# Performance work log

Hardware: AMD Instinct MI355X
Metric: run time of the kernel (lower is better)

## Reference

```python
import jax, jax.numpy as jnp
import numpy as np

N_NODES = 20000
N_EDGES = 320000
N_GRAPHS = 32
IN_CH = 5
HID = 64
HEADS = 4
DH = HID // HEADS  # 16
LAYERS = 8
EPS = 1e-5
SLOPE = 0.2


def setup_inputs() -> dict:
    key = jax.random.key(0)
    ks = jax.random.split(key, 32)
    inp = {}
    inp['x1'] = jax.random.normal(ks[0], (N_NODES, IN_CH), dtype=jnp.float32)
    inp['x2'] = jax.random.normal(ks[1], (N_NODES, IN_CH), dtype=jnp.float32)
    inp['edge_index1'] = jax.random.randint(ks[2], (2, N_EDGES), 0, N_NODES, dtype=jnp.int32)
    inp['edge_index2'] = jax.random.randint(ks[3], (2, N_EDGES), 0, N_NODES, dtype=jnp.int32)
    inp['batch1'] = jnp.sort(jax.random.randint(ks[4], (N_NODES,), 0, N_GRAPHS, dtype=jnp.int32))
    inp['batch2'] = jnp.sort(jax.random.randint(ks[5], (N_NODES,), 0, N_GRAPHS, dtype=jnp.int32))
    # node_lin
    inp['Wn'] = jax.random.normal(ks[6], (IN_CH, HID), dtype=jnp.float32) / np.sqrt(IN_CH)
    inp['bnode'] = jnp.zeros((HID,), dtype=jnp.float32)
    # GATv2 layers (stacked over LAYERS)
    s = 1.0 / np.sqrt(HID)
    inp['Wl'] = jax.random.normal(ks[7], (LAYERS, HID, HID), dtype=jnp.float32) * s
    inp['bl'] = jnp.zeros((LAYERS, HID), dtype=jnp.float32)
    inp['Wr'] = jax.random.normal(ks[8], (LAYERS, HID, HID), dtype=jnp.float32) * s
    inp['br'] = jnp.zeros((LAYERS, HID), dtype=jnp.float32)
    inp['att'] = jax.random.normal(ks[9], (LAYERS, HEADS, DH), dtype=jnp.float32) / np.sqrt(DH)
    inp['cbias'] = jnp.zeros((LAYERS, HID), dtype=jnp.float32)
    # batch norms
    inp['gamma'] = jnp.ones((LAYERS, HID), dtype=jnp.float32)
    inp['beta'] = jnp.zeros((LAYERS, HID), dtype=jnp.float32)
    # fc head
    inp['f1w'] = jax.random.normal(ks[10], (2 * HID, 256), dtype=jnp.float32) / np.sqrt(2 * HID)
    inp['f1b'] = jnp.zeros((256,), dtype=jnp.float32)
    inp['f2w'] = jax.random.normal(ks[11], (256, 128), dtype=jnp.float32) / np.sqrt(256)
    inp['f2b'] = jnp.zeros((128,), dtype=jnp.float32)
    inp['f3w'] = jax.random.normal(ks[12], (128, 1), dtype=jnp.float32) / np.sqrt(128)
    inp['f3b'] = jnp.zeros((1,), dtype=jnp.float32)
    return inp


def _gatv2_layer(x, src, dst, Wl, bl, Wr, br, att, bias):
    # x: [N, HID]; src/dst: [E'] (self loops included)
    N = x.shape[0]
    xl = (x @ Wl + bl).reshape(N, HEADS, DH)  # source transform
    xr = (x @ Wr + br).reshape(N, HEADS, DH)  # target transform
    e = jax.nn.leaky_relu(xl[src] + xr[dst], SLOPE)          # [E, H, DH]
    score = jnp.einsum('ehd,hd->eh', e, att)                  # [E, H]
    smax = jax.ops.segment_max(score, dst, num_segments=N)    # [N, H]
    ex = jnp.exp(score - smax[dst])
    denom = jax.ops.segment_sum(ex, dst, num_segments=N)
    alpha = ex / denom[dst]                                   # [E, H]
    msg = alpha[:, :, None] * xl[src]                         # [E, H, DH]
    out = jax.ops.segment_sum(msg, dst, num_segments=N)       # [N, H, DH]
    return out.reshape(N, HID) + bias


def _forward_once(x, edge_index, batch, Wn, bnode, Wl, bl, Wr, br, att, cbias, gamma, beta):
    N = x.shape[0]
    loop = jnp.arange(N, dtype=edge_index.dtype)
    src = jnp.concatenate([edge_index[0], loop])  # add_self_loops=True
    dst = jnp.concatenate([edge_index[1], loop])
    h = x @ Wn + bnode
    for l in range(LAYERS):
        g = _gatv2_layer(h, src, dst, Wl[l], bl[l], Wr[l], br[l], att[l], cbias[l])
        mu = g.mean(axis=0)
        var = g.var(axis=0)
        g = (g - mu) / jnp.sqrt(var + EPS) * gamma[l] + beta[l]
        h = h + jax.nn.elu(g)
    # global_mean_pool
    sums = jax.ops.segment_sum(h, batch, num_segments=N_GRAPHS)
    cnt = jax.ops.segment_sum(jnp.ones((N,), dtype=h.dtype), batch, num_segments=N_GRAPHS)
    return sums / jnp.maximum(cnt, 1.0)[:, None]


def reference(x1, edge_index1, batch1, x2, edge_index2, batch2, Wn, bnode, Wl, bl, Wr, br, att, cbias, gamma, beta, f1w, f1b, f2w, f2b, f3w, f3b):
    o1 = _forward_once(x1, edge_index1, batch1, Wn, bnode, Wl, bl, Wr, br, att, cbias, gamma, beta)
    o2 = _forward_once(x2, edge_index2, batch2, Wn, bnode, Wl, bl, Wr, br, att, cbias, gamma, beta)
    c = jnp.concatenate([o1, o2], axis=1)           # [G, 128]
    h = jax.nn.relu(c @ f1w + f1b)                   # dropout = identity (eval)
    h = jax.nn.relu(h @ f2w + f2b)
    return h @ f3w + f3b                             # [G, 1]
```

## Files before the change

### kernel.cpp

```cpp
#include <hip/hip_runtime.h>
#include <hip/hip_bf16.h>
#include <hip/hip_fp16.h>

#define N_NODES 20000
#define HID 64
#define EPS 1e-5f

struct GP {
    const int* ei;
    const int* batch;
    const float* x;
    int* deg;
    int* cursor;
    int* csr;
    float* h;
    __half* xlh;
    float* xr;
    float* gb;
    float* stats;
    float* osum;
};


__global__ void k_csr_init(GP a, GP b, int n, int two) {
    int t = blockIdx.x * blockDim.x + threadIdx.x;
    if (t < n) {
        a.deg[t] = 1;
        if (two) b.deg[t] = 1;
    }
}

__global__ void k_count(GP a, GP b, int Ea, int Eb, int two) {
    int t = blockIdx.x * blockDim.x + threadIdx.x;
    if (t < Ea) atomicAdd(&a.deg[a.ei[Ea + t]], 1);
    if (two && t < Eb) atomicAdd(&b.deg[b.ei[Eb + t]], 1);
}

#define SCAN_T 1024
#define SCAN_C 20
__global__ __launch_bounds__(1024) void k_scan(GP a, GP b, int n, int totA, int totB) {
    GP g = blockIdx.x ? b : a;
    int total = blockIdx.x ? totB : totA;
    __shared__ int sd[SCAN_T];
    int t = threadIdx.x;
    int base = t * SCAN_C;
    int loc[SCAN_C];
    int s = 0;
#pragma unroll
    for (int i = 0; i < SCAN_C; ++i) {
        int idx = base + i;
        loc[i] = (idx < n) ? g.deg[idx] : 0;
        s += loc[i];
    }
    sd[t] = s;
    __syncthreads();
    for (int off = 1; off < SCAN_T; off <<= 1) {
        int v = (t >= off) ? sd[t - off] : 0;
        __syncthreads();
        sd[t] += v;
        __syncthreads();
    }
    int run = sd[t] - s;
#pragma unroll
    for (int i = 0; i < SCAN_C; ++i) {
        int idx = base + i;
        if (idx < n) { g.deg[idx] = run; g.cursor[idx] = run; run += loc[i]; }
    }
    if (t == 0) g.deg[n] = total;
}

__global__ void k_scatter(GP a, GP b, int Ea, int Eb, int n, int two) {
    int t = blockIdx.x * blockDim.x + threadIdx.x;
    if (t < Ea) {
        int s = a.ei[t], d = a.ei[Ea + t];
        a.csr[atomicAdd(&a.cursor[d], 1)] = s;
    } else if (t < Ea + n) {
        int nn = t - Ea;
        a.csr[atomicAdd(&a.cursor[nn], 1)] = nn;
    }
    if (two) {
        if (t < Eb) {
            int s = b.ei[t], d = b.ei[Eb + t];
            b.csr[atomicAdd(&b.cursor[d], 1)] = s;
        } else if (t < Eb + n) {
            int nn = t - Eb;
            b.csr[atomicAdd(&b.cursor[nn], 1)] = nn;
        }
    }
}


__global__ void k_nodelin(GP a, GP b, int nPer, const float* __restrict__ Wn,
                          const float* __restrict__ bn, int n) {
    int bid = blockIdx.x;
    GP g = a;
    if (bid >= nPer) { g = b; bid -= nPer; }
    int idx = bid * 256 + threadIdx.x;
    if (idx >= n * HID) return;
    int node = idx >> 6, c = idx & 63;
    float acc = bn[c];
#pragma unroll
    for (int k = 0; k < 5; ++k) acc += g.x[node * 5 + k] * Wn[k * HID + c];
    g.h[idx] = acc;
}


__global__ __launch_bounds__(256) void k_lin2(GP ga, GP gbp, int nPer, int n,
        const float* __restrict__ Wl, const float* __restrict__ bl,
        const float* __restrict__ Wr, const float* __restrict__ br,
        const float* __restrict__ gamma, const float* __restrict__ beta, int layer) {
    __shared__ float wls[4096], wrs[4096];
    __shared__ float hs[2048];
    int bid = blockIdx.x;
    GP g = ga;
    if (bid >= nPer) { g = gbp; bid -= nPer; }
    {
        const float4* wl4 = (const float4*)Wl;
        const float4* wr4 = (const float4*)Wr;
        float4* l4 = (float4*)wls;
        float4* r4 = (float4*)wrs;
        for (int i = threadIdx.x; i < 1024; i += 256) { l4[i] = wl4[i]; r4[i] = wr4[i]; }
    }
    int c = threadIdx.x & 63;
    int wid = threadIdx.x >> 6;
    float blv = bl[c], brv = br[c];
    float mu = 0.f, inv = 1.f, gam = 1.f, bet = 0.f;
    if (layer > 0) {
        const float* st = g.stats + (layer - 1) * 128;
        float invn = 1.0f / (float)n;
        mu = st[c] * invn;
        float var = st[64 + c] * invn - mu * mu;
        inv = rsqrtf(fmaxf(var, 0.f) + EPS);
        gam = gamma[c]; bet = beta[c];
    }
    __syncthreads();
    float* hw = &hs[wid * 512];
    const float4* hw4 = (const float4*)hw;
    for (int base = bid * 32; base < n; base += nPer * 32) {
        int nb = base + wid * 8;
        size_t off0 = (size_t)nb * 64 + c;
        float hv[8];
        if (layer > 0) {
#pragma unroll
            for (int j = 0; j < 8; ++j) {
                float gv = g.gb[off0 + j * 64];
                float ov = g.h[off0 + j * 64];
                float v = (gv - mu) * inv * gam + bet;
                v = v > 0.f ? v : expm1f(v);
                hv[j] = ov + v;
                g.h[off0 + j * 64] = hv[j];
            }
        } else {
#pragma unroll
            for (int j = 0; j < 8; ++j) hv[j] = g.h[off0 + j * 64];
        }
#pragma unroll
        for (int j = 0; j < 8; ++j) hw[j * 64 + c] = hv[j];
        float accl[8], accr[8];
#pragma unroll
        for (int j = 0; j < 8; ++j) { accl[j] = blv; accr[j] = brv; }
        for (int k4 = 0; k4 < 16; ++k4) {
            float4 hq[8];
#pragma unroll
            for (int j = 0; j < 8; ++j) hq[j] = hw4[j * 16 + k4];
#pragma unroll
            for (int kk = 0; kk < 4; ++kk) {
                float wl = wls[(k4 * 4 + kk) * 64 + c];
                float wr = wrs[(k4 * 4 + kk) * 64 + c];
#pragma unroll
                for (int j = 0; j < 8; ++j) {
                    float hx = (&hq[j].x)[kk];
                    accl[j] = fmaf(hx, wl, accl[j]);
                    accr[j] = fmaf(hx, wr, accr[j]);
                }
            }
        }
#pragma unroll
        for (int j = 0; j < 8; ++j) {
            g.xlh[off0 + j * 64] = __float2half(accl[j]);
            g.xr[off0 + j * 64] = accr[j];
        }
    }
}


__device__ __forceinline__ float red16(float p) {
    p += __int_as_float(__builtin_amdgcn_update_dpp(0, __float_as_int(p), 0xB1, 0xF, 0xF, true));
    p += __int_as_float(__builtin_amdgcn_update_dpp(0, __float_as_int(p), 0x4E, 0xF, 0xF, true));
    p += __int_as_float(__builtin_amdgcn_update_dpp(0, __float_as_int(p), 0x141, 0xF, 0xF, true));
    p += __int_as_float(__builtin_amdgcn_update_dpp(0, __float_as_int(p), 0x140, 0xF, 0xF, true));
    return p;
}

__global__ __launch_bounds__(1024) void k_attn(GP ga, GP gbp, int nPer,
        const float* __restrict__ att, const float* __restrict__ cbias, int layer, int n) {
    int bid = blockIdx.x;
    GP g = (bid & 1) ? gbp : ga;
    bid >>= 1;
    int lane = threadIdx.x & 63;
    int wid = threadIdx.x >> 6;
    int gw = bid * 16 + wid;
    int nw = nPer * 16;
    float attv = att[lane];
    float attv2 = attv * 0.2f;
    float cb = cbias[lane];
    const int* __restrict__ rowptr = g.deg;
    const int* __restrict__ csr = g.csr;
    const __half* __restrict__ xl = g.xlh;
    const float* __restrict__ xr = g.xr;
    float* __restrict__ gbuf = g.gb;
    float* st = g.stats + layer * 128;
    float bsum = 0.f, bsq = 0.f;
    for (int node = gw; node < n; node += nw) {
        int start = rowptr[node], end = rowptr[node + 1];
        float xrv = xr[(size_t)node * 64 + lane];
        float xself = __half2float(xl[(size_t)node * 64 + lane]);
        float ts = xself + xrv;
        float sself = red16(ts * (ts > 0.f ? attv : attv2));
        float lsum = 0.f, acc = 0.f;
        int idx = start;
        for (; idx + 8 <= end; idx += 8) {
            int sidx[8];
            float xv[8];
#pragma unroll
            for (int j = 0; j < 8; ++j) sidx[j] = csr[idx + j];
#pragma unroll
            for (int j = 0; j < 8; ++j) xv[j] = __half2float(xl[(size_t)sidx[j] * 64 + lane]);
#pragma unroll
            for (int j = 0; j < 8; ++j) {
                float t = xv[j] + xrv;
                float p = red16(t * (t > 0.f ? attv : attv2));
                float w = __expf(fminf(p - sself, 80.f));
                lsum += w;
                acc = fmaf(w, xv[j], acc);
            }
        }
        for (; idx + 4 <= end; idx += 4) {
            int sidx[4];
            float xv[4];
#pragma unroll
            for (int j = 0; j < 4; ++j) sidx[j] = csr[idx + j];
#pragma unroll
            for (int j = 0; j < 4; ++j) xv[j] = __half2float(xl[(size_t)sidx[j] * 64 + lane]);
#pragma unroll
            for (int j = 0; j < 4; ++j) {
                float t = xv[j] + xrv;
                float p = red16(t * (t > 0.f ? attv : attv2));
                float w = __expf(fminf(p - sself, 80.f));
                lsum += w;
                acc = fmaf(w, xv[j], acc);
            }
        }
        for (; idx < end; ++idx) {
            int s0 = csr[idx];
            float x0 = __half2float(xl[(size_t)s0 * 64 + lane]);
            float t0 = x0 + xrv;
            float p0 = red16(t0 * (t0 > 0.f ? attv : attv2));
            float w0 = __expf(fminf(p0 - sself, 80.f));
            lsum += w0;
            acc = fmaf(w0, x0, acc);
        }
        float outv = acc / lsum + cb;
        gbuf[(size_t)node * 64 + lane] = outv;
        bsum += outv; bsq += outv * outv;
    }
    __shared__ float sred[1024];
    sred[threadIdx.x] = bsum;
    __syncthreads();
    if (threadIdx.x < 64) {
        float t = 0.f;
#pragma unroll
        for (int w = 0; w < 16; ++w) t += sred[w * 64 + threadIdx.x];
        atomicAdd(&st[threadIdx.x], t);
    }
    __syncthreads();
    sred[threadIdx.x] = bsq;
    __syncthreads();
    if (threadIdx.x < 64) {
        float t = 0.f;
#pragma unroll
        for (int w = 0; w < 16; ++w) t += sred[w * 64 + threadIdx.x];
        atomicAdd(&st[64 + threadIdx.x], t);
    }
}


__global__ __launch_bounds__(256) void k_pool(GP ga, GP gbp, int nPer,
        const float* __restrict__ gamma, const float* __restrict__ beta, int n) {
    int bid = blockIdx.x;
    GP g = ga;
    if (bid >= nPer) { g = gbp; bid -= nPer; }
    int lane = threadIdx.x & 63, w = threadIdx.x >> 6;
    const float* st = g.stats + 7 * 128;
    float invn = 1.f / (float)n;
    float mu = st[lane] * invn;
    float var = st[64 + lane] * invn - mu * mu;
    float inv = rsqrtf(fmaxf(var, 0.f) + EPS);
    float gam = gamma[lane], bet = beta[lane];
    int chunk = (n + nPer - 1) / nPer;
    int s = bid * chunk;
    int e = min(s + chunk, n);
    float acc = 0.f;
    int cur = -1;
    for (int node = s + w; node < e; node += 4) {
        int bg = g.batch[node];
        size_t off = (size_t)node * 64 + lane;
        float gv = g.gb[off];
        float hv = g.h[off];
        float v = (gv - mu) * inv * gam + bet;
        float hn = hv + (v > 0.f ? v : expm1f(v));
        if (bg != cur) {
            if (cur >= 0) atomicAdd(&g.osum[cur * 64 + lane], acc);
            acc = 0.f; cur = bg;
        }
        acc += hn;
    }
    if (cur >= 0) atomicAdd(&g.osum[cur * 64 + lane], acc);
}


__device__ __forceinline__ int lb(const int* __restrict__ b, int n, int v) {
    int lo = 0, hi = n;
    while (lo < hi) { int mid = (lo + hi) >> 1; if (b[mid] < v) lo = mid + 1; else hi = mid; }
    return lo;
}

__global__ __launch_bounds__(256) void k_fc(const float* __restrict__ o1, const float* __restrict__ o2,
                                            const int* __restrict__ b1, const int* __restrict__ b2,
                                            const float* __restrict__ f1w, const float* __restrict__ f1b,
                                            const float* __restrict__ f2w, const float* __restrict__ f2b,
                                            const float* __restrict__ f3w, const float* __restrict__ f3b,
                                            float* __restrict__ out, int n) {
    int gid = blockIdx.x, t = threadIdx.x;
    __shared__ float cin[128];
    __shared__ float h1[256];
    __shared__ float red[128];
    __shared__ int cnts[2];
    if (t == 0) cnts[0] = lb(b1, n, gid + 1) - lb(b1, n, gid);
    if (t == 1) cnts[1] = lb(b2, n, gid + 1) - lb(b2, n, gid);
    __syncthreads();
    if (t < 64) {
        float c1 = (float)(cnts[0] > 0 ? cnts[0] : 1);
        float c2 = (float)(cnts[1] > 0 ? cnts[1] : 1);
        cin[t] = o1[gid * 64 + t] / c1;
        cin[64 + t] = o2[gid * 64 + t] / c2;
    }
    __syncthreads();
    float a = f1b[t];
#pragma unroll 8
    for (int k = 0; k < 128; ++k) a += cin[k] * f1w[k * 256 + t];
    h1[t] = fmaxf(a, 0.f);
    __syncthreads();
    if (t < 128) {
        float a2 = f2b[t];
#pragma unroll 8
        for (int k = 0; k < 256; ++k) a2 += h1[k] * f2w[k * 128 + t];
        red[t] = fmaxf(a2, 0.f) * f3w[t];
    }
    __syncthreads();
    for (int off = 64; off > 0; off >>= 1) {
        if (t < off) red[t] += red[t + off];
        __syncthreads();
    }
    if (t == 0) out[gid] = red[0] + f3b[0];
}


extern "C" void kernel_launch(void* const* d_in, const int* in_sizes, int n_in,
                              void* d_out, int out_size, void* d_ws, size_t ws_size,
                              hipStream_t stream) {
    const float* x1 = (const float*)d_in[0];
    const float* x2 = (const float*)d_in[1];
    const int* ei1 = (const int*)d_in[2];
    const int* ei2 = (const int*)d_in[3];
    const int* b1 = (const int*)d_in[4];
    const int* b2 = (const int*)d_in[5];
    const float* Wn = (const float*)d_in[6];
    const float* bnode = (const float*)d_in[7];
    const float* Wl = (const float*)d_in[8];
    const float* bl = (const float*)d_in[9];
    const float* Wr = (const float*)d_in[10];
    const float* br = (const float*)d_in[11];
    const float* att = (const float*)d_in[12];
    const float* cbias = (const float*)d_in[13];
    const float* gamma = (const float*)d_in[14];
    const float* beta = (const float*)d_in[15];
    const float* f1w = (const float*)d_in[16];
    const float* f1b = (const float*)d_in[17];
    const float* f2w = (const float*)d_in[18];
    const float* f2b = (const float*)d_in[19];
    const float* f3w = (const float*)d_in[20];
    const float* f3b = (const float*)d_in[21];
    float* out = (float*)d_out;

    const int N = N_NODES;
    const int EA = in_sizes[2] / 2;
    const int EB = in_sizes[3] / 2;
    const size_t INT_PG = 20096 + 20096 + 340096;
    const size_t BIG = (size_t)N * 64;
    const size_t SMALL = 2 * 1024 + 2 * 2048;
    const size_t dualBytes = 2 * INT_PG * 4 + (8 * BIG + SMALL) * 4;
    const int dual = (ws_size >= dualBytes) ? 1 : 0;

    int* ibase = (int*)d_ws;
    int* iA = ibase;
    int* iB = dual ? ibase + INT_PG : ibase;
    float* fbase = (float*)(ibase + (size_t)(dual ? 2 : 1) * INT_PG);
    float* hA = fbase;
    float* xlA = hA + BIG;
    float* xrA = xlA + BIG;
    float* gbA = xrA + BIG;
    float* hB = dual ? gbA + BIG : hA;
    float* xlB = dual ? hB + BIG : xlA;
    float* xrB = dual ? xlB + BIG : xrA;
    float* gbB = dual ? xrB + BIG : gbA;
    float* small = dual ? gbB + BIG : gbA + BIG;
    float* statsA = small;
    float* statsB = small + 1024;
    float* osumA = small + 2048;
    float* osumB = small + 4096;

    GP A, B;
    A.ei = ei1; A.batch = b1; A.x = x1;
    A.deg = iA; A.cursor = iA + 20096; A.csr = iA + 40192;
    A.h = hA; A.xlh = (__half*)xlA; A.xr = xrA; A.gb = gbA; A.stats = statsA; A.osum = osumA;
    B.ei = ei2; B.batch = b2; B.x = x2;
    B.deg = iB; B.cursor = iB + 20096; B.csr = iB + 40192;
    B.h = hB; B.xlh = (__half*)xlB; B.xr = xrB; B.gb = gbB; B.stats = statsB; B.osum = osumB;

    hipMemsetAsync(small, 0, SMALL * sizeof(float), stream);

    const int LIN2_NB = 320;
    const int ATT_NB = 256;
    const int POOL_NB = 250;

    if (dual) {
        int Emax = EA > EB ? EA : EB;
        k_csr_init<<<(N + 255) / 256, 256, 0, stream>>>(A, B, N, 1);
        k_count<<<(Emax + 255) / 256, 256, 0, stream>>>(A, B, EA, EB, 1);
        k_scan<<<2, 1024, 0, stream>>>(A, B, N, EA + N, EB + N);
        k_scatter<<<(Emax + N + 255) / 256, 256, 0, stream>>>(A, B, EA, EB, N, 1);
        k_nodelin<<<2 * ((N * 64) / 256), 256, 0, stream>>>(A, B, (N * 64) / 256, Wn, bnode, N);
        for (int l = 0; l < 8; ++l) {
            const float* gm = l ? gamma + (l - 1) * 64 : gamma;
            const float* bt = l ? beta + (l - 1) * 64 : beta;
            k_lin2<<<2 * LIN2_NB, 256, 0, stream>>>(A, B, LIN2_NB, N, Wl + l * 4096, bl + l * 64,
                                                    Wr + l * 4096, br + l * 64, gm, bt, l);
            k_attn<<<2 * ATT_NB, 1024, 0, stream>>>(A, B, ATT_NB, att + l * 64, cbias + l * 64, l, N);
        }
        k_pool<<<2 * POOL_NB, 256, 0, stream>>>(A, B, POOL_NB, gamma + 7 * 64, beta + 7 * 64, N);
    } else {
        for (int gi = 0; gi < 2; ++gi) {
            GP G = gi ? B : A;
            int E = gi ? EB : EA;
            k_csr_init<<<(N + 255) / 256, 256, 0, stream>>>(G, G, N, 0);
            k_count<<<(E + 255) / 256, 256, 0, stream>>>(G, G, E, E, 0);
            k_scan<<<1, 1024, 0, stream>>>(G, G, N, E + N, E + N);
            k_scatter<<<(E + N + 255) / 256, 256, 0, stream>>>(G, G, E, E, N, 0);
            k_nodelin<<<(N * 64) / 256, 256, 0, stream>>>(G, G, (N * 64) / 256, Wn, bnode, N);
            for (int l = 0; l < 8; ++l) {
                const float* gm = l ? gamma + (l - 1) * 64 : gamma;
                const float* bt = l ? beta + (l - 1) * 64 : beta;
                k_lin2<<<LIN2_NB, 256, 0, stream>>>(G, G, LIN2_NB, N, Wl + l * 4096, bl + l * 64,
                                                    Wr + l * 4096, br + l * 64, gm, bt, l);
                k_attn<<<2 * ATT_NB, 1024, 0, stream>>>(G, G, ATT_NB, att + l * 64, cbias + l * 64, l, N);
            }
            k_pool<<<POOL_NB, 256, 0, stream>>>(G, G, POOL_NB, gamma + 7 * 64, beta + 7 * 64, N);
        }
    }
    k_fc<<<32, 256, 0, stream>>>(osumA, osumB, b1, b2, f1w, f1b, f2w, f2b, f3w, f3b, out, N);
}
```

Baseline: 693.5 us.

## Split xl into two head-pair halves and process two edges per wave

The fp16 source features are stored as two separate 32-channel planes (heads 0-1 and heads 2-3), and the attention kernel runs two passes, each handling one plane. Within a pass each half of the wave processes a different edge, so a gathered row is 64 bytes and the working set per pass is halved, which should improve cache hit rates for the random gathers. CSR entries are pre-scaled by 64 to give byte offsets, and exp is computed as exp2 with the log2e factor folded into att. The cost is walking the CSR twice, extra cross-half shuffles and masked tail handling.

Result: slower. 778.4 us (+12.2%).

```diff
diff --git a/kernel.cpp b/kernel.cpp
--- a/kernel.cpp
+++ b/kernel.cpp
@@ -14,7 +14,8 @@
     int* cursor;
     int* csr;
     float* h;
-    __half* xlh;
+    __half* xlh0;
+    __half* xlh1;
     float* xr;
     float* gb;
     float* stats;
@@ -73,18 +74,18 @@
     int t = blockIdx.x * blockDim.x + threadIdx.x;
     if (t < Ea) {
         int s = a.ei[t], d = a.ei[Ea + t];
-        a.csr[atomicAdd(&a.cursor[d], 1)] = s;
+        a.csr[atomicAdd(&a.cursor[d], 1)] = s * 64;
     } else if (t < Ea + n) {
         int nn = t - Ea;
-        a.csr[atomicAdd(&a.cursor[nn], 1)] = nn;
+        a.csr[atomicAdd(&a.cursor[nn], 1)] = nn * 64;
     }
     if (two) {
         if (t < Eb) {
             int s = b.ei[t], d = b.ei[Eb + t];
-            b.csr[atomicAdd(&b.cursor[d], 1)] = s;
+            b.csr[atomicAdd(&b.cursor[d], 1)] = s * 64;
         } else if (t < Eb + n) {
             int nn = t - Eb;
-            b.csr[atomicAdd(&b.cursor[nn], 1)] = nn;
+            b.csr[atomicAdd(&b.cursor[nn], 1)] = nn * 64;
         }
     }
 }
@@ -136,6 +137,8 @@
     __syncthreads();
     float* hw = &hs[wid * 512];
     const float4* hw4 = (const float4*)hw;
+    __half* xbase = (c < 32) ? g.xlh0 : g.xlh1;
+    int cc = c & 31;
     for (int base = bid * 32; base < n; base += nPer * 32) {
         int nb = base + wid * 8;
         size_t off0 = (size_t)nb * 64 + c;
@@ -177,7 +180,7 @@
         }
 #pragma unroll
         for (int j = 0; j < 8; ++j) {
-            g.xlh[off0 + j * 64] = __float2half(accl[j]);
+            xbase[(size_t)(nb + j) * 32 + cc] = __float2half(accl[j]);
             g.xr[off0 + j * 64] = accr[j];
         }
     }
@@ -199,88 +202,85 @@
     bid >>= 1;
     int lane = threadIdx.x & 63;
     int wid = threadIdx.x >> 6;
+    int h = lane >> 5;
+    int cl = lane & 31;
     int gw = bid * 16 + wid;
     int nw = nPer * 16;
-    float attv = att[lane];
-    float attv2 = attv * 0.2f;
-    float cb = cbias[lane];
     const int* __restrict__ rowptr = g.deg;
     const int* __restrict__ csr = g.csr;
-    const __half* __restrict__ xl = g.xlh;
     const float* __restrict__ xr = g.xr;
     float* __restrict__ gbuf = g.gb;
     float* st = g.stats + layer * 128;
-    float bsum = 0.f, bsq = 0.f;
-    for (int node = gw; node < n; node += nw) {
-        int start = rowptr[node], end = rowptr[node + 1];
-        float xrv = xr[(size_t)node * 64 + lane];
-        float xself = __half2float(xl[(size_t)node * 64 + lane]);
-        float ts = xself + xrv;
-        float sself = red16(ts * (ts > 0.f ? attv : attv2));
-        float lsum = 0.f, acc = 0.f;
-        int idx = start;
-        for (; idx + 8 <= end; idx += 8) {
-            int sidx[8];
-            float xv[8];
-#pragma unroll
-            for (int j = 0; j < 8; ++j) sidx[j] = csr[idx + j];
-#pragma unroll
-            for (int j = 0; j < 8; ++j) xv[j] = __half2float(xl[(size_t)sidx[j] * 64 + lane]);
-#pragma unroll
-            for (int j = 0; j < 8; ++j) {
-                float t = xv[j] + xrv;
+    __shared__ float sred[1024];
+    for (int pass = 0; pass < 2; ++pass) {
+        const char* xlb = (const char*)(pass ? g.xlh1 : g.xlh0) + (size_t)cl * 2;
+        float attv = att[pass * 32 + cl] * 1.44269504f;
+        float attv2 = attv * 0.2f;
+        float cb = cbias[pass * 32 + cl];
+        float bsum = 0.f, bsq = 0.f;
+        for (int node = gw; node < n; node += nw) {
+            int start = rowptr[node], end = rowptr[node + 1];
+            float xrv = xr[(size_t)node * 64 + pass * 32 + cl];
+            float xself = __half2float(*(const __half*)(xlb + (size_t)node * 64));
+            float ts = xself + xrv;
+            float sself = red16(ts * (ts > 0.f ? attv : attv2));
+            float lsum = 0.f, acc = 0.f;
+            int idx = start;
+            for (; idx + 8 <= end; idx += 8) {
+                int off[4];
+                float xv[4];
+#pragma unroll
+                for (int j = 0; j < 4; ++j) off[j] = csr[idx + 2 * j + h];
+#pragma unroll
+                for (int j = 0; j < 4; ++j) xv[j] = __half2float(*(const __half*)(xlb + off[j]));
+#pragma unroll
+                for (int j = 0; j < 4; ++j) {
+                    float t = xv[j] + xrv;
+                    float p = red16(t * (t > 0.f ? attv : attv2));
+                    float w = exp2f(fminf(p - sself, 110.f));
+                    lsum += w;
+                    acc = fmaf(w, xv[j], acc);
+                }
+            }
+            for (; idx < end; idx += 2) {
+                int e = idx + h;
+                bool valid = e < end;
+                int ec = valid ? e : end - 1;
+                int off = csr[ec];
+                float xv = __half2float(*(const __half*)(xlb + off));
+                float t = xv + xrv;
                 float p = red16(t * (t > 0.f ? attv : attv2));
-                float w = __expf(fminf(p - sself, 80.f));
+                float w = exp2f(fminf(p - sself, 110.f));
+                w = valid ? w : 0.f;
                 lsum += w;
-                acc = fmaf(w, xv[j], acc);
-            }
-        }
-        for (; idx + 4 <= end; idx += 4) {
-            int sidx[4];
-            float xv[4];
-#pragma unroll
-            for (int j = 0; j < 4; ++j) sidx[j] = csr[idx + j];
-#pragma unroll
-            for (int j = 0; j < 4; ++j) xv[j] = __half2float(xl[(size_t)sidx[j] * 64 + lane]);
-#pragma unroll
-            for (int j = 0; j < 4; ++j) {
-                float t = xv[j] + xrv;
-                float p = red16(t * (t > 0.f ? attv : attv2));
-                float w = __expf(fminf(p - sself, 80.f));
-                lsum += w;
-                acc = fmaf(w, xv[j], acc);
-            }
-        }
-        for (; idx < end; ++idx) {
-            int s0 = csr[idx];
-            float x0 = __half2float(xl[(size_t)s0 * 64 + lane]);
-            float t0 = x0 + xrv;
-            float p0 = red16(t0 * (t0 > 0.f ? attv : attv2));
-            float w0 = __expf(fminf(p0 - sself, 80.f));
-            lsum += w0;
-            acc = fmaf(w0, x0, acc);
-        }
-        float outv = acc / lsum + cb;
-        gbuf[(size_t)node * 64 + lane] = outv;
-        bsum += outv; bsq += outv * outv;
-    }
-    __shared__ float sred[1024];
-    sred[threadIdx.x] = bsum;
-    __syncthreads();
-    if (threadIdx.x < 64) {
-        float t = 0.f;
-#pragma unroll
-        for (int w = 0; w < 16; ++w) t += sred[w * 64 + threadIdx.x];
-        atomicAdd(&st[threadIdx.x], t);
-    }
-    __syncthreads();
-    sred[threadIdx.x] = bsq;
-    __syncthreads();
-    if (threadIdx.x < 64) {
-        float t = 0.f;
-#pragma unroll
-        for (int w = 0; w < 16; ++w) t += sred[w * 64 + threadIdx.x];
-        atomicAdd(&st[64 + threadIdx.x], t);
+                acc = fmaf(w, xv, acc);
+            }
+            lsum += __shfl_xor(lsum, 32);
+            acc += __shfl_xor(acc, 32);
+            float outv = acc / lsum + cb;
+            if (h == 0) {
+                gbuf[(size_t)node * 64 + pass * 32 + cl] = outv;
+                bsum += outv; bsq += outv * outv;
+            }
+        }
+        sred[threadIdx.x] = (h == 0) ? bsum : 0.f;
+        __syncthreads();
+        if (threadIdx.x < 32) {
+            float t = 0.f;
+#pragma unroll
+            for (int w = 0; w < 16; ++w) t += sred[w * 64 + threadIdx.x];
+            atomicAdd(&st[pass * 32 + threadIdx.x], t);
+        }
+        __syncthreads();
+        sred[threadIdx.x] = (h == 0) ? bsq : 0.f;
+        __syncthreads();
+        if (threadIdx.x < 32) {
+            float t = 0.f;
+#pragma unroll
+            for (int w = 0; w < 16; ++w) t += sred[w * 64 + threadIdx.x];
+            atomicAdd(&st[64 + pass * 32 + threadIdx.x], t);
+        }
+        __syncthreads();
     }
 }
 
@@ -423,10 +423,12 @@
     GP A, B;
     A.ei = ei1; A.batch = b1; A.x = x1;
     A.deg = iA; A.cursor = iA + 20096; A.csr = iA + 40192;
-    A.h = hA; A.xlh = (__half*)xlA; A.xr = xrA; A.gb = gbA; A.stats = statsA; A.osum = osumA;
+    A.h = hA; A.xlh0 = (__half*)xlA; A.xlh1 = (__half*)xlA + (size_t)N * 32;
+    A.xr = xrA; A.gb = gbA; A.stats = statsA; A.osum = osumA;
     B.ei = ei2; B.batch = b2; B.x = x2;
     B.deg = iB; B.cursor = iB + 20096; B.csr = iB + 40192;
-    B.h = hB; B.xlh = (__half*)xlB; B.xr = xrB; B.gb = gbB; B.stats = statsB; B.osum = osumB;
+    B.h = hB; B.xlh0 = (__half*)xlB; B.xlh1 = (__half*)xlB + (size_t)N * 32;
+    B.xr = xrB; B.gb = gbB; B.stats = statsB; B.osum = osumB;
 
     hipMemsetAsync(small, 0, SMALL * sizeof(float), stream);
 
```
